# Kernel optimization log

Measured on AMD Instinct MI355X. Metric: run time of the kernel, lower is better.

Reference implementation:

```python
import jax, jax.numpy as jnp
import numpy as np

_EPS = 1e-8

# Stacked Sobel kernels, pre-divided by 8 (matches conv2d(...)/8.0 in torch).
# Shape: (O=2, I=1, 3, 3); channel 0 = sobel_x, channel 1 = sobel_y.
_SOBEL = jnp.stack([
    jnp.array([[-1.0, 0.0, 1.0], [-2.0, 0.0, 2.0], [-1.0, 0.0, 1.0]], jnp.float32),
    jnp.array([[-1.0, -2.0, -1.0], [0.0, 0.0, 0.0], [1.0, 2.0, 1.0]], jnp.float32),
])[:, None, :, :] / 8.0


def setup_inputs() -> dict:
    key = jax.random.key(0)
    k1, k2 = jax.random.split(key)
    B, C, H, W = 64, 1, 512, 512
    pred_dist = jax.random.uniform(k1, (B, C, H, W), dtype=jnp.float32) * 10.0
    reachable = jax.random.uniform(k2, (B, C, H, W), dtype=jnp.float32)
    return {"pred_dist": pred_dist, "reachable": reachable}


def reference(pred_dist, reachable) -> jnp.ndarray:
    # Replicate (edge) padding, as F.pad(..., mode='replicate')
    padded = jnp.pad(pred_dist, ((0, 0), (0, 0), (1, 1), (1, 1)), mode="edge")
    # Single conv with 2 output channels computes grad_x and grad_y together.
    grads = jax.lax.conv_general_dilated(
        padded, _SOBEL.astype(pred_dist.dtype),
        window_strides=(1, 1), padding="VALID",
        dimension_numbers=("NCHW", "OIHW", "NCHW"),
    )  # [B, 2, H, W]
    gx = grads[:, 0:1]
    gy = grads[:, 1:2]
    magnitude = jnp.sqrt(gx * gx + gy * gy + _EPS)
    violation = jnp.abs(magnitude - 1.0)
    mask = (reachable > 0.5).astype(violation.dtype)
    denom = jnp.maximum(mask.sum(), 1.0)
    return (violation * mask).sum() / denom
```

## Files before the change

kernel.cpp:

```cpp
#include <hip/hip_runtime.h>
#include <math.h>

#define HW   512
#define IMG  (512 * 512)
#define NB   64
#define T    4
#define BLOCK 256
#define WAVES_PER_BLOCK (BLOCK / 64)
#define WAVES_PER_IMG (HW / T)
#define TOTAL_WAVES (NB * WAVES_PER_IMG)
#define NBLOCKS     (TOTAL_WAVES / WAVES_PER_BLOCK)

__device__ __forceinline__ void unpack8(const float4& q0, const float4& q1, float* a) {
    a[0] = q0.x; a[1] = q0.y; a[2] = q0.z; a[3] = q0.w;
    a[4] = q1.x; a[5] = q1.y; a[6] = q1.z; a[7] = q1.w;
}

__global__ __launch_bounds__(BLOCK) void eik_main(const float* __restrict__ pred,
                                                  const float* __restrict__ reach,
                                                  float* __restrict__ partials) {
    const int lane = threadIdx.x & 63;
    const int w    = blockIdx.x * WAVES_PER_BLOCK + (threadIdx.x >> 6);
    const int y0   = (w & (WAVES_PER_IMG - 1)) * T;
    const int b    = w >> 7;
    const int xo   = lane << 3;

    const float* base = pred + (size_t)b * IMG;

    float4 P[6][2];
#pragma unroll
    for (int j = 0; j < 6; ++j) {
        int r = y0 - 1 + j;
        r = r < 0 ? 0 : (r > HW - 1 ? HW - 1 : r);
        const float* p = base + (size_t)r * HW + xo;
        P[j][0] = *(const float4*)p;
        P[j][1] = *(const float4*)(p + 4);
    }
    float4 R[T][2];
    const float* rbase = reach + (size_t)b * IMG + (size_t)y0 * HW + xo;
#pragma unroll
    for (int t = 0; t < T; ++t) {
        R[t][0] = *(const float4*)(rbase + (size_t)t * HW);
        R[t][1] = *(const float4*)(rbase + (size_t)t * HW + 4);
    }

    float vsum = 0.0f, csum = 0.0f;

#pragma unroll
    for (int t = 0; t < T; ++t) {
        float am[8], a0[8], ap[8], rv[8];
        unpack8(P[t][0],     P[t][1],     am);
        unpack8(P[t + 1][0], P[t + 1][1], a0);
        unpack8(P[t + 2][0], P[t + 2][1], ap);
        unpack8(R[t][0],     R[t][1],     rv);

        float s[8], d[8];
#pragma unroll
        for (int i = 0; i < 8; ++i) {
            s[i] = am[i] + 2.0f * a0[i] + ap[i];
            d[i] = ap[i] - am[i];
        }

        float sl = __shfl_up(s[7], 1, 64);
        float dl = __shfl_up(d[7], 1, 64);
        float sr = __shfl_down(s[0], 1, 64);
        float dr = __shfl_down(d[0], 1, 64);
        if (lane == 0)  { sl = s[0]; dl = d[0]; }
        if (lane == 63) { sr = s[7]; dr = d[7]; }

        const float S[10] = {sl, s[0], s[1], s[2], s[3], s[4], s[5], s[6], s[7], sr};
        const float D[10] = {dl, d[0], d[1], d[2], d[3], d[4], d[5], d[6], d[7], dr};

#pragma unroll
        for (int i = 0; i < 8; ++i) {
            const float gx = (S[i+2] - S[i]) * 0.125f;
            const float gy = (D[i] + 2.0f * D[i+1] + D[i+2]) * 0.125f;
            const float mag  = __builtin_amdgcn_sqrtf(gx * gx + gy * gy + 1e-8f);
            const float viol = fabsf(mag - 1.0f);
            const bool  m    = rv[i] > 0.5f;
            vsum += m ? viol : 0.0f;
            csum += m ? 1.0f : 0.0f;
        }
    }

#pragma unroll
    for (int off = 32; off > 0; off >>= 1) {
        vsum += __shfl_down(vsum, off, 64);
        csum += __shfl_down(csum, off, 64);
    }

    __shared__ float sv[WAVES_PER_BLOCK];
    __shared__ float sc[WAVES_PER_BLOCK];
    const int wid = threadIdx.x >> 6;
    if (lane == 0) { sv[wid] = vsum; sc[wid] = csum; }
    __syncthreads();
    if (threadIdx.x == 0) {
        partials[2 * blockIdx.x]     = sv[0] + sv[1] + sv[2] + sv[3];
        partials[2 * blockIdx.x + 1] = sc[0] + sc[1] + sc[2] + sc[3];
    }
}

__global__ __launch_bounds__(BLOCK) void eik_finalize(const float* __restrict__ partials,
                                                      float* __restrict__ out) {
    float v = 0.0f, c = 0.0f;
    for (int i = threadIdx.x; i < NBLOCKS; i += BLOCK) {
        v += partials[2 * i];
        c += partials[2 * i + 1];
    }
#pragma unroll
    for (int off = 32; off > 0; off >>= 1) {
        v += __shfl_down(v, off, 64);
        c += __shfl_down(c, off, 64);
    }
    __shared__ float sv[WAVES_PER_BLOCK];
    __shared__ float sc[WAVES_PER_BLOCK];
    const int lane = threadIdx.x & 63;
    const int wid  = threadIdx.x >> 6;
    if (lane == 0) { sv[wid] = v; sc[wid] = c; }
    __syncthreads();
    if (threadIdx.x == 0) {
        const float vt = sv[0] + sv[1] + sv[2] + sv[3];
        const float ct = sc[0] + sc[1] + sc[2] + sc[3];
        out[0] = vt / fmaxf(ct, 1.0f);
    }
}

extern "C" void kernel_launch(void* const* d_in, const int* in_sizes, int n_in,
                              void* d_out, int out_size, void* d_ws, size_t ws_size,
                              hipStream_t stream) {
    const float* pred  = (const float*)d_in[0];
    const float* reach = (const float*)d_in[1];
    float* out = (float*)d_out;
    float* ws  = (float*)d_ws;

    eik_main<<<NBLOCKS, BLOCK, 0, stream>>>(pred, reach, ws);
    eik_finalize<<<1, BLOCK, 0, stream>>>(ws, out);
}
```

Baseline: 146.6 us.

## Stage 16-row strips through LDS with direct global-to-LDS loads

Each block now owns a 16-row strip of one image and copies pred and reachable rows into shared memory with global_load_lds. Each wave then reads its four rows plus halo from LDS, so only the strip edges fetch extra halo rows from global memory. The aim is to cut redundant halo reads from global memory and make the loads asynchronous. The cost is 64KB of LDS per block, which limits occupancy to about two blocks per CU, and a block-wide barrier.

Result: no change. 146.9 us (+0.2%).

```diff
diff --git a/kernel.cpp b/kernel.cpp
--- a/kernel.cpp
+++ b/kernel.cpp
@@ -4,50 +4,87 @@
 #define HW   512
 #define IMG  (512 * 512)
 #define NB   64
-#define T    4
+#define SR   16
 #define BLOCK 256
 #define WAVES_PER_BLOCK (BLOCK / 64)
-#define WAVES_PER_IMG (HW / T)
-#define TOTAL_WAVES (NB * WAVES_PER_IMG)
-#define NBLOCKS     (TOTAL_WAVES / WAVES_PER_BLOCK)
+#define STRIPS_PER_IMG (HW / SR)
+#define NBLOCKS (NB * STRIPS_PER_IMG)
 
 __device__ __forceinline__ void unpack8(const float4& q0, const float4& q1, float* a) {
     a[0] = q0.x; a[1] = q0.y; a[2] = q0.z; a[3] = q0.w;
     a[4] = q1.x; a[5] = q1.y; a[6] = q1.z; a[7] = q1.w;
 }
 
-__global__ __launch_bounds__(BLOCK) void eik_main(const float* __restrict__ pred,
-                                                  const float* __restrict__ reach,
-                                                  float* __restrict__ partials) {
+__device__ __forceinline__ void gload_lds16(const float* g, float* l) {
+    __builtin_amdgcn_global_load_lds(
+        (const __attribute__((address_space(1))) void*)g,
+        (__attribute__((address_space(3))) void*)l,
+        16, 0, 0);
+}
+
+__global__ __launch_bounds__(BLOCK, 2) void eik_main(const float* __restrict__ pred,
+                                                     const float* __restrict__ reach,
+                                                     float* __restrict__ partials) {
     const int lane = threadIdx.x & 63;
-    const int w    = blockIdx.x * WAVES_PER_BLOCK + (threadIdx.x >> 6);
-    const int y0   = (w & (WAVES_PER_IMG - 1)) * T;
-    const int b    = w >> 7;
-    const int xo   = lane << 3;
+    const int w    = threadIdx.x >> 6;
+    const int strip = blockIdx.x & (STRIPS_PER_IMG - 1);
+    const int b     = blockIdx.x >> 5;
+    const int y0    = strip * SR;
 
-    const float* base = pred + (size_t)b * IMG;
+    __shared__ float smem[2 * SR * HW];
 
+    const float* pbase = pred  + (size_t)b * IMG + (size_t)y0 * HW;
+    const float* rbase = reach + (size_t)b * IMG + (size_t)y0 * HW;
+
+    float4 H0 = {}, H1 = {};
+    if (w == 0) {
+        const int hy = (y0 == 0) ? 0 : -1;
+        const float* hp = pbase + hy * HW + (lane << 3);
+        H0 = *(const float4*)hp;
+        H1 = *(const float4*)(hp + 4);
+    }
+    if (w == 3) {
+        const int hy = (y0 + SR > HW - 1) ? (SR - 1) : SR;
+        const float* hp = pbase + hy * HW + (lane << 3);
+        H0 = *(const float4*)hp;
+        H1 = *(const float4*)(hp + 4);
+    }
+
+#pragma unroll
+    for (int k = 0; k < 16; ++k) {
+        const int u = (w << 4) | k;
+        const float* src = (u < 32)
+            ? pbase + (size_t)(u >> 1) * HW        + ((u & 1) << 8) + (lane << 2)
+            : rbase + (size_t)((u - 32) >> 1) * HW + ((u & 1) << 8) + (lane << 2);
+        gload_lds16(src, smem + u * 256);
+    }
+
+    __syncthreads();
+
+    const int r0 = w << 2;
     float4 P[6][2];
+    float4 R[4][2];
 #pragma unroll
     for (int j = 0; j < 6; ++j) {
-        int r = y0 - 1 + j;
-        r = r < 0 ? 0 : (r > HW - 1 ? HW - 1 : r);
-        const float* p = base + (size_t)r * HW + xo;
+        int sr = r0 - 1 + j;
+        sr = sr < 0 ? 0 : (sr > SR - 1 ? SR - 1 : sr);
+        const float* p = smem + sr * HW + (lane << 3);
         P[j][0] = *(const float4*)p;
         P[j][1] = *(const float4*)(p + 4);
     }
-    float4 R[T][2];
-    const float* rbase = reach + (size_t)b * IMG + (size_t)y0 * HW + xo;
 #pragma unroll
-    for (int t = 0; t < T; ++t) {
-        R[t][0] = *(const float4*)(rbase + (size_t)t * HW);
-        R[t][1] = *(const float4*)(rbase + (size_t)t * HW + 4);
+    for (int t = 0; t < 4; ++t) {
+        const float* p = smem + SR * HW + (r0 + t) * HW + (lane << 3);
+        R[t][0] = *(const float4*)p;
+        R[t][1] = *(const float4*)(p + 4);
     }
+    if (w == 0) { P[0][0] = H0; P[0][1] = H1; }
+    if (w == 3) { P[5][0] = H0; P[5][1] = H1; }
 
     float vsum = 0.0f, csum = 0.0f;
 
 #pragma unroll
-    for (int t = 0; t < T; ++t) {
+    for (int t = 0; t < 4; ++t) {
         float am[8], a0[8], ap[8], rv[8];
         unpack8(P[t][0],     P[t][1],     am);
         unpack8(P[t + 1][0], P[t + 1][1], a0);
@@ -91,8 +128,7 @@
 
     __shared__ float sv[WAVES_PER_BLOCK];
     __shared__ float sc[WAVES_PER_BLOCK];
-    const int wid = threadIdx.x >> 6;
-    if (lane == 0) { sv[wid] = vsum; sc[wid] = csum; }
+    if (lane == 0) { sv[w] = vsum; sc[w] = csum; }
     __syncthreads();
     if (threadIdx.x == 0) {
         partials[2 * blockIdx.x]     = sv[0] + sv[1] + sv[2] + sv[3];
```
